# Kernel tuning notes

Measured on AMD Instinct MI355X. Metric: run time of the kernel, lower is better.

Reference implementation:

```python
import jax, jax.numpy as jnp
import numpy as np

N_CAT, IN, H, OUT = 1024, 1024, 2048, 32000


def _lstm_cell(x, h, c, w_ih, w_hh, b_ih, b_hh):
    # x: [1, D], h/c: [1, H]; PyTorch gate order: i, f, g, o
    gates = x @ w_ih.T + b_ih + h @ w_hh.T + b_hh  # [1, 4H]
    i, f, g, o = jnp.split(gates, 4, axis=-1)
    i = jax.nn.sigmoid(i)
    f = jax.nn.sigmoid(f)
    g = jnp.tanh(g)
    o = jax.nn.sigmoid(o)
    c_new = f * c + i * g
    h_new = o * jnp.tanh(c_new)
    return h_new, c_new


def setup_inputs() -> dict:
    key = jax.random.key(0)
    ks = jax.random.split(key, 16)
    s = 0.02
    return {
        "category": jax.random.normal(ks[0], (1, N_CAT), jnp.float32),
        "input": jax.random.normal(ks[1], (1, IN), jnp.float32),
        "hidden": jax.random.normal(ks[2], (2, 1, H), jnp.float32),
        "cell_state": jax.random.normal(ks[3], (2, 1, H), jnp.float32),
        # LSTM layer 0: input dim = N_CAT + IN
        "w_ih_l0": jax.random.normal(ks[4], (4 * H, N_CAT + IN), jnp.float32) * s,
        "w_hh_l0": jax.random.normal(ks[5], (4 * H, H), jnp.float32) * s,
        "b_ih_l0": jax.random.normal(ks[6], (4 * H,), jnp.float32) * s,
        "b_hh_l0": jax.random.normal(ks[7], (4 * H,), jnp.float32) * s,
        # LSTM layer 1: input dim = H
        "w_ih_l1": jax.random.normal(ks[8], (4 * H, H), jnp.float32) * s,
        "w_hh_l1": jax.random.normal(ks[9], (4 * H, H), jnp.float32) * s,
        "b_ih_l1": jax.random.normal(ks[10], (4 * H,), jnp.float32) * s,
        "b_hh_l1": jax.random.normal(ks[11], (4 * H,), jnp.float32) * s,
        # output linear: [OUT, N_CAT + H]
        "w_out": jax.random.normal(ks[12], (OUT, N_CAT + H), jnp.float32) * s,
        "b_out": jax.random.normal(ks[13], (OUT,), jnp.float32) * s,
    }


def reference(category, input, hidden, cell_state,
              w_ih_l0, w_hh_l0, b_ih_l0, b_hh_l0,
              w_ih_l1, w_hh_l1, b_ih_l1, b_hh_l1,
              w_out, b_out):
    # single-step, batch=1, seq=1; dropout layers are identity (eval mode)
    x = jnp.concatenate([category, input], axis=-1)  # [1, N_CAT+IN]
    h1, c1 = _lstm_cell(x, hidden[0], cell_state[0], w_ih_l0, w_hh_l0, b_ih_l0, b_hh_l0)
    h2, c2 = _lstm_cell(h1, hidden[1], cell_state[1], w_ih_l1, w_hh_l1, b_ih_l1, b_hh_l1)
    out_comb = jnp.concatenate([category, h2], axis=-1)  # [1, N_CAT+H]
    logits = out_comb @ w_out.T + b_out  # [1, OUT]
    logp = jax.nn.log_softmax(logits, axis=1)
    new_hidden = jnp.stack([h1, h2], axis=0)      # [2, 1, H]
    new_cell = jnp.stack([c1, c2], axis=0)        # [2, 1, H]
    return logp, new_hidden, new_cell
```

## Files before the change

### kernel.cpp

```cpp
#include <hip/hip_runtime.h>
#include <math.h>

#define HDIM 2048
#define OUTN 32000
#define KOUT 3072
#define NPART 2000

__device__ __forceinline__ float wave_reduce_sum(float v) {
    #pragma unroll
    for (int off = 32; off > 0; off >>= 1)
        v += __shfl_down(v, off, 64);
    return v;
}

__device__ __forceinline__ float dot4(float4 a, float4 b) {
    return a.x * b.x + a.y * b.y + a.z * b.z + a.w * b.w;
}

typedef float nfloat4 __attribute__((ext_vector_type(4)));
__device__ __forceinline__ float4 ldnt4(const float4* p) {
    nfloat4 v = __builtin_nontemporal_load((const nfloat4*)p);
    return make_float4(v.x, v.y, v.z, v.w);
}

__device__ __forceinline__ float sigmoidf_(float x) {
    return 1.0f / (1.0f + __expf(-x));
}

__global__ __launch_bounds__(256) void lstm_kernel(
    const float* __restrict__ xa,
    const float* __restrict__ xb,
    const float* __restrict__ h,
    const float* __restrict__ c,
    const float* __restrict__ w_ih,
    const float* __restrict__ w_hh,
    const float* __restrict__ b_ih,
    const float* __restrict__ b_hh,
    float* __restrict__ h_out,
    float* __restrict__ c_out)
{
    const int wave = threadIdx.x >> 6;
    const int lane = threadIdx.x & 63;
    const int n0   = blockIdx.x * 2;
    const int row0 = n0 + wave * HDIM;

    const float4* wi0 = (const float4*)(w_ih + (size_t)row0 * HDIM);
    const float4* wh0 = (const float4*)(w_hh + (size_t)row0 * HDIM);
    const float4* xa4 = (const float4*)xa;
    const float4* xb4 = (const float4*)xb;
    const float4* h4  = (const float4*)h;

    float a0 = 0.f, a1 = 0.f;
    #pragma unroll
    for (int it = 0; it < 8; ++it) {
        const int k4 = it * 64 + lane;
        float4 xv = (it < 4) ? xa4[k4] : xb4[k4 - 256];
        float4 hv = h4[k4];
        a0 += dot4(ldnt4(&wi0[k4]),       xv) + dot4(ldnt4(&wh0[k4]),       hv);
        a1 += dot4(ldnt4(&wi0[k4 + 512]), xv) + dot4(ldnt4(&wh0[k4 + 512]), hv);
    }
    a0 = wave_reduce_sum(a0);
    a1 = wave_reduce_sum(a1);

    __shared__ float sg[4][2];
    if (lane == 0) {
        sg[wave][0] = a0 + b_ih[row0]     + b_hh[row0];
        sg[wave][1] = a1 + b_ih[row0 + 1] + b_hh[row0 + 1];
    }
    __syncthreads();

    if (threadIdx.x < 2) {
        const int t  = threadIdx.x;
        float gi = sigmoidf_(sg[0][t]);
        float gf = sigmoidf_(sg[1][t]);
        float gg = tanhf(sg[2][t]);
        float go = sigmoidf_(sg[3][t]);
        float cn = gf * c[n0 + t] + gi * gg;
        float hn = go * tanhf(cn);
        c_out[n0 + t] = cn;
        h_out[n0 + t] = hn;
    }
}

__global__ __launch_bounds__(256) void logits_kernel(
    const float* __restrict__ cat,
    const float* __restrict__ h2,
    const float* __restrict__ w_out,
    const float* __restrict__ b_out,
    float* __restrict__ logits,
    float2* __restrict__ partial)
{
    const int wave = threadIdx.x >> 6;
    const int lane = threadIdx.x & 63;
    const int row0 = blockIdx.x * 16 + wave * 4;

    const float4* w4 = (const float4*)(w_out + (size_t)row0 * KOUT);
    const float4* c4 = (const float4*)cat;
    const float4* h4 = (const float4*)h2;

    float a0 = 0.f, a1 = 0.f, a2 = 0.f, a3 = 0.f;
    #pragma unroll
    for (int it = 0; it < 12; ++it) {
        const int k4 = it * 64 + lane;
        float4 v = (it < 4) ? c4[k4] : h4[k4 - 256];
        a0 += dot4(ldnt4(&w4[k4]),        v);
        a1 += dot4(ldnt4(&w4[k4 + 768]),  v);
        a2 += dot4(ldnt4(&w4[k4 + 1536]), v);
        a3 += dot4(ldnt4(&w4[k4 + 2304]), v);
    }
    a0 = wave_reduce_sum(a0);
    a1 = wave_reduce_sum(a1);
    a2 = wave_reduce_sum(a2);
    a3 = wave_reduce_sum(a3);

    __shared__ float sm[4], ss[4];
    if (lane == 0) {
        a0 += b_out[row0];
        a1 += b_out[row0 + 1];
        a2 += b_out[row0 + 2];
        a3 += b_out[row0 + 3];
        *(float4*)(logits + row0) = make_float4(a0, a1, a2, a3);
        float m = fmaxf(fmaxf(a0, a1), fmaxf(a2, a3));
        float s = __expf(a0 - m) + __expf(a1 - m) + __expf(a2 - m) + __expf(a3 - m);
        sm[wave] = m; ss[wave] = s;
    }
    __syncthreads();
    if (threadIdx.x == 0) {
        float M = sm[0], S = ss[0];
        #pragma unroll
        for (int w = 1; w < 4; ++w) {
            float mn = fmaxf(M, sm[w]);
            S = S * __expf(M - mn) + ss[w] * __expf(sm[w] - mn);
            M = mn;
        }
        partial[blockIdx.x] = make_float2(M, S);
    }
}

__global__ __launch_bounds__(1024) void lse_combine(
    const float2* __restrict__ partial, float* __restrict__ logz)
{
    float m = -INFINITY, s = 0.f;
    for (int i = threadIdx.x; i < NPART; i += 1024) {
        float2 p  = partial[i];
        float  mn = fmaxf(m, p.x);
        s = s * __expf(m - mn) + p.y * __expf(p.x - mn);
        m = mn;
    }
    #pragma unroll
    for (int off = 32; off > 0; off >>= 1) {
        float m2 = __shfl_down(m, off, 64);
        float s2 = __shfl_down(s, off, 64);
        float mn = fmaxf(m, m2);
        s = s * __expf(m - mn) + s2 * __expf(m2 - mn);
        m = mn;
    }
    __shared__ float smm[16], sss[16];
    const int wave = threadIdx.x >> 6;
    const int lane = threadIdx.x & 63;
    if (lane == 0) { smm[wave] = m; sss[wave] = s; }
    __syncthreads();
    if (threadIdx.x == 0) {
        float M = smm[0], S = sss[0];
        for (int w = 1; w < 16; ++w) {
            float mn = fmaxf(M, smm[w]);
            S = S * __expf(M - mn) + sss[w] * __expf(smm[w] - mn);
            M = mn;
        }
        *logz = M + logf(S);
    }
}

__global__ __launch_bounds__(256) void sub_kernel(
    const float* __restrict__ logits, const float* __restrict__ logz,
    float* __restrict__ out)
{
    const int i = blockIdx.x * 256 + threadIdx.x;
    out[i] = logits[i] - *logz;
}

extern "C" void kernel_launch(void* const* d_in, const int* in_sizes, int n_in,
                              void* d_out, int out_size, void* d_ws, size_t ws_size,
                              hipStream_t stream) {
    const float* category = (const float*)d_in[0];
    const float* input    = (const float*)d_in[1];
    const float* hidden   = (const float*)d_in[2];
    const float* cell     = (const float*)d_in[3];
    const float* w_ih_l0  = (const float*)d_in[4];
    const float* w_hh_l0  = (const float*)d_in[5];
    const float* b_ih_l0  = (const float*)d_in[6];
    const float* b_hh_l0  = (const float*)d_in[7];
    const float* w_ih_l1  = (const float*)d_in[8];
    const float* w_hh_l1  = (const float*)d_in[9];
    const float* b_ih_l1  = (const float*)d_in[10];
    const float* b_hh_l1  = (const float*)d_in[11];
    const float* w_out    = (const float*)d_in[12];
    const float* b_out    = (const float*)d_in[13];

    float* out  = (float*)d_out;
    float* logp = out;
    float* h1   = out + OUTN;
    float* h2   = out + OUTN + HDIM;
    float* c1   = out + OUTN + 2 * HDIM;
    float* c2   = out + OUTN + 3 * HDIM;

    float* logits = (float*)d_ws;
    float* logz   = logits + OUTN;
    float2* partial = (float2*)logp;

    lstm_kernel<<<HDIM / 2, 256, 0, stream>>>(category, input,
                                              hidden, cell,
                                              w_ih_l0, w_hh_l0, b_ih_l0, b_hh_l0,
                                              h1, c1);
    lstm_kernel<<<HDIM / 2, 256, 0, stream>>>(h1, h1 + 1024,
                                              hidden + HDIM, cell + HDIM,
                                              w_ih_l1, w_hh_l1, b_ih_l1, b_hh_l1,
                                              h2, c2);
    logits_kernel<<<NPART, 256, 0, stream>>>(category, h2, w_out, b_out,
                                             logits, partial);
    lse_combine<<<1, 1024, 0, stream>>>(partial, logz);
    sub_kernel<<<OUTN / 256, 256, 0, stream>>>(logits, logz, logp);
}
```

Baseline: 649.3 us.

## Split LSTM into contiguous-row GEMV and separate pointwise gate kernel

Each wave now computes four consecutive gate rows with contiguous weight streams, instead of two rows per block spread across the four gate slices. The gate activations move into a separate small pointwise kernel that reads the gate vector from workspace. This removes the in-block shared-memory sync and cross-gate coupling and gives more independent loads per wave. The cost is two extra kernel launches plus a workspace round-trip of the gate vectors.

```diff
diff --git a/kernel.cpp b/kernel.cpp
--- a/kernel.cpp
+++ b/kernel.cpp
@@ -27,59 +27,76 @@
     return 1.0f / (1.0f + __expf(-x));
 }
 
-__global__ __launch_bounds__(256) void lstm_kernel(
+__global__ __launch_bounds__(256) void lstm_gemv(
     const float* __restrict__ xa,
     const float* __restrict__ xb,
     const float* __restrict__ h,
-    const float* __restrict__ c,
     const float* __restrict__ w_ih,
     const float* __restrict__ w_hh,
     const float* __restrict__ b_ih,
     const float* __restrict__ b_hh,
-    float* __restrict__ h_out,
-    float* __restrict__ c_out)
+    float* __restrict__ gates)
 {
     const int wave = threadIdx.x >> 6;
     const int lane = threadIdx.x & 63;
-    const int n0   = blockIdx.x * 2;
-    const int row0 = n0 + wave * HDIM;
-
-    const float4* wi0 = (const float4*)(w_ih + (size_t)row0 * HDIM);
-    const float4* wh0 = (const float4*)(w_hh + (size_t)row0 * HDIM);
+    const int g    = blockIdx.x * 4 + wave;
+    const int r0   = g * 4;
+
+    const float4* wi  = (const float4*)(w_ih + (size_t)r0 * HDIM);
+    const float4* wh  = (const float4*)(w_hh + (size_t)r0 * HDIM);
     const float4* xa4 = (const float4*)xa;
     const float4* xb4 = (const float4*)xb;
     const float4* h4  = (const float4*)h;
 
-    float a0 = 0.f, a1 = 0.f;
+    float a0 = 0.f, a1 = 0.f, a2 = 0.f, a3 = 0.f;
     #pragma unroll
     for (int it = 0; it < 8; ++it) {
         const int k4 = it * 64 + lane;
         float4 xv = (it < 4) ? xa4[k4] : xb4[k4 - 256];
+        a0 += dot4(ldnt4(&wi[k4]),        xv);
+        a1 += dot4(ldnt4(&wi[k4 + 512]),  xv);
+        a2 += dot4(ldnt4(&wi[k4 + 1024]), xv);
+        a3 += dot4(ldnt4(&wi[k4 + 1536]), xv);
+    }
+    #pragma unroll
+    for (int it = 0; it < 8; ++it) {
+        const int k4 = it * 64 + lane;
         float4 hv = h4[k4];
-        a0 += dot4(ldnt4(&wi0[k4]),       xv) + dot4(ldnt4(&wh0[k4]),       hv);
-        a1 += dot4(ldnt4(&wi0[k4 + 512]), xv) + dot4(ldnt4(&wh0[k4 + 512]), hv);
+        a0 += dot4(ldnt4(&wh[k4]),        hv);
+        a1 += dot4(ldnt4(&wh[k4 + 512]),  hv);
+        a2 += dot4(ldnt4(&wh[k4 + 1024]), hv);
+        a3 += dot4(ldnt4(&wh[k4 + 1536]), hv);
     }
     a0 = wave_reduce_sum(a0);
     a1 = wave_reduce_sum(a1);
-
-    __shared__ float sg[4][2];
+    a2 = wave_reduce_sum(a2);
+    a3 = wave_reduce_sum(a3);
+
     if (lane == 0) {
-        sg[wave][0] = a0 + b_ih[row0]     + b_hh[row0];
-        sg[wave][1] = a1 + b_ih[row0 + 1] + b_hh[row0 + 1];
-    }
-    __syncthreads();
-
-    if (threadIdx.x < 2) {
-        const int t  = threadIdx.x;
-        float gi = sigmoidf_(sg[0][t]);
-        float gf = sigmoidf_(sg[1][t]);
-        float gg = tanhf(sg[2][t]);
-        float go = sigmoidf_(sg[3][t]);
-        float cn = gf * c[n0 + t] + gi * gg;
-        float hn = go * tanhf(cn);
-        c_out[n0 + t] = cn;
-        h_out[n0 + t] = hn;
-    }
+        float4 bi = ((const float4*)b_ih)[g];
+        float4 bh = ((const float4*)b_hh)[g];
+        ((float4*)gates)[g] = make_float4(a0 + bi.x + bh.x,
+                                          a1 + bi.y + bh.y,
+                                          a2 + bi.z + bh.z,
+                                          a3 + bi.w + bh.w);
+    }
+}
+
+__global__ __launch_bounds__(256) void lstm_point(
+    const float* __restrict__ gates,
+    const float* __restrict__ c,
+    float* __restrict__ h_out,
+    float* __restrict__ c_out)
+{
+    const int n = blockIdx.x * 256 + threadIdx.x;
+    float gi = sigmoidf_(gates[n]);
+    float gf = sigmoidf_(gates[HDIM + n]);
+    float gg = tanhf(gates[2 * HDIM + n]);
+    float go = sigmoidf_(gates[3 * HDIM + n]);
+    float cn = gf * c[n] + gi * gg;
+    float hn = go * tanhf(cn);
+    c_out[n] = cn;
+    h_out[n] = hn;
 }
 
 __global__ __launch_bounds__(256) void logits_kernel(
@@ -204,18 +221,20 @@
     float* c1   = out + OUTN + 2 * HDIM;
     float* c2   = out + OUTN + 3 * HDIM;
 
-    float* logits = (float*)d_ws;
+    float* gates  = (float*)d_ws;
+    float* logits = gates + 4 * HDIM;
     float* logz   = logits + OUTN;
     float2* partial = (float2*)logp;
 
-    lstm_kernel<<<HDIM / 2, 256, 0, stream>>>(category, input,
-                                              hidden, cell,
-                                              w_ih_l0, w_hh_l0, b_ih_l0, b_hh_l0,
-                                              h1, c1);
-    lstm_kernel<<<HDIM / 2, 256, 0, stream>>>(h1, h1 + 1024,
-                                              hidden + HDIM, cell + HDIM,
-                                              w_ih_l1, w_hh_l1, b_ih_l1, b_hh_l1,
-                                              h2, c2);
+    lstm_gemv<<<512, 256, 0, stream>>>(category, input, hidden,
+                                       w_ih_l0, w_hh_l0, b_ih_l0, b_hh_l0,
+                                       gates);
+    lstm_point<<<8, 256, 0, stream>>>(gates, cell, h1, c1);
+    lstm_gemv<<<512, 256, 0, stream>>>(h1, h1 + 1024, hidden + HDIM,
+                                       w_ih_l1, w_hh_l1, b_ih_l1, b_hh_l1,
+                                       gates);
+    lstm_point<<<8, 256, 0, stream>>>(gates, cell + HDIM, h2, c2);
+
     logits_kernel<<<NPART, 256, 0, stream>>>(category, h2, w_out, b_out,
                                              logits, partial);
     lse_combine<<<1, 1024, 0, stream>>>(partial, logz);
```

After: 652.3 us. No clear change (+0.5%).
